# Kernel tuning notes

Hardware: AMD Instinct MI355X
Metric: run time of the kernel (lower is better)

Reference implementation:

```python
import jax, jax.numpy as jnp
import numpy as np

WINDOW = 7
EPS = 1e-8


def setup_inputs() -> dict:
    key = jax.random.key(0)
    k1, k2, k3 = jax.random.split(key, 3)
    x = jax.random.normal(k1, (8, 256, 64, 64), dtype=jnp.float32)
    # 1x1 conv weights (bias=False): [out_ch, in_ch]
    w_reduce = jax.random.normal(k2, (64, 256), dtype=jnp.float32) * 0.05
    w_proj = jax.random.normal(k3, (512, 64), dtype=jnp.float32) * 0.1
    return {"x": x, "w_reduce": w_reduce, "w_proj": w_proj}


def _unfold_window(feat, window):
    # feat: [b, c, h, w] -> patches: [b, c, window*window, h, w]
    b, c, h, w = feat.shape
    pad = window // 2
    fp = jnp.pad(feat, ((0, 0), (0, 0), (pad, pad), (pad, pad)))
    # fixed small loop over window^2 = 49 shifts (matches F.unfold ordering)
    return jnp.stack(
        [fp[:, :, i:i + h, j:j + w] for i in range(window) for j in range(window)],
        axis=2,
    )


def reference(x, w_reduce, w_proj):
    window = WINDOW
    # reduce: 1x1 conv, no bias
    feat = jnp.einsum('oc,bchw->bohw', w_reduce, x)  # [b, cr, h, w]
    patches = _unfold_window(feat, window)           # [b, cr, K, h, w], K=49
    # cosine similarity between center feature and each window patch (dim=channel)
    dot = jnp.einsum('bchw,bckhw->bkhw', feat, patches)          # [b, K, h, w]
    cn = jnp.sqrt(jnp.sum(feat * feat, axis=1))                  # [b, h, w]
    pn = jnp.sqrt(jnp.sum(patches * patches, axis=1))            # [b, K, h, w]
    sim = dot / jnp.maximum(cn[:, None] * pn, EPS)               # [b, K, h, w]
    att = jax.nn.softmax(sim, axis=1)                            # softmax over window dim
    corr = jnp.einsum('bkhw,bckhw->bchw', att, patches)          # [b, cr, h, w]
    # proj: 1x1 conv, no bias
    return jnp.einsum('oc,bchw->bohw', w_proj, corr)             # [b, out, h, w]
```

## Files before the change

### kernel.cpp

```cpp
#include <hip/hip_runtime.h>
#include <stdint.h>

#define NPIX 4096
#define CIN  256
#define CR   64
#define COUT 512
#define NB   8
#define CG   256
#define FT   128

typedef _Float16 half8 __attribute__((ext_vector_type(8)));
typedef _Float16 half4 __attribute__((ext_vector_type(4)));
typedef _Float16 half2v __attribute__((ext_vector_type(2)));
typedef float f32x4 __attribute__((ext_vector_type(4)));

__device__ __forceinline__ float dpp8_sum(float d) {
  int y;
  y = __builtin_amdgcn_update_dpp(0, __float_as_int(d), 0xB1, 0xF, 0xF, true);
  d += __int_as_float(y);
  y = __builtin_amdgcn_update_dpp(0, __float_as_int(d), 0x4E, 0xF, 0xF, true);
  d += __int_as_float(y);
  y = __builtin_amdgcn_update_dpp(0, __float_as_int(d), 0x141, 0xF, 0xF, true);
  d += __int_as_float(y);
  return d;
}

__global__ __launch_bounds__(256) void k0_prep(
    const float* __restrict__ wr, const float* __restrict__ wp,
    _Float16* __restrict__ wrAh, _Float16* __restrict__ wrAl,
    _Float16* __restrict__ wpH,
    float* __restrict__ icnG, float* __restrict__ featTail)
{
  const int tid = blockIdx.x * 256 + threadIdx.x;
  if (tid < 16384) {
    const int j = tid & 7, l = (tid >> 3) & 63;
    const int kt = (tid >> 9) & 7, mt = tid >> 12;
    const int m = mt * 16 + (l & 15);
    const int k = kt * 32 + (l >> 4) * 8 + j;
    const float v = wr[m * CIN + k];
    const _Float16 h = (_Float16)v;
    wrAh[tid] = h;
    wrAl[tid] = (_Float16)(v - (float)h);
  } else if (tid < 16384 + COUT * CR) {
    const int fi = tid - 16384;
    const int j = fi & 7, l = (fi >> 3) & 63;
    const int kt = (fi >> 9) & 1, ot = (fi >> 10) & 3, g = fi >> 12;
    const int o = g * 64 + ot * 16 + (l & 15);
    const int k = kt * 32 + (l >> 4) * 8 + j;
    wpH[fi] = (_Float16)wp[o * CR + k];
  } else {
    const int gi = tid - (16384 + COUT * CR);
    if (gi < CG)               icnG[gi] = 0.f;
    else if (gi < 2 * CG)      icnG[CG + NB * NPIX + (gi - CG)] = 0.f;
    else if (gi < 2 * CG + FT) featTail[gi - 2 * CG] = 0.f;
  }
}

__global__ __launch_bounds__(512) void k1_reduce(
    const float* __restrict__ x,
    const _Float16* __restrict__ wrAh, const _Float16* __restrict__ wrAl,
    _Float16* __restrict__ feat_h, float* __restrict__ icn)
{
  const int blk = blockIdx.x;
  const int b = blk >> 6, seg = blk & 63;
  const int t = threadIdx.x, lane = t & 63;
  const int g = __builtin_amdgcn_readfirstlane((int)t >> 6);
  const int nt = g & 3, mth = g >> 2;
  const int col = lane & 15, krow = lane >> 4;

  const float* xb = x + (size_t)b * CIN * NPIX + seg * 64 + nt * 16 + col;

  f32x4 c0 = {0.f, 0.f, 0.f, 0.f};
  f32x4 c1 = {0.f, 0.f, 0.f, 0.f};

#pragma unroll
  for (int kt = 0; kt < 8; ++kt) {
    half8 Bh, Bl;
    const float* xk = xb + (size_t)(kt * 32 + krow * 8) * NPIX;
#pragma unroll
    for (int j = 0; j < 8; ++j) {
      const float v = xk[(size_t)j * NPIX];
      const _Float16 h = (_Float16)v;
      Bh[j] = h;
      Bl[j] = (_Float16)(v - (float)h);
    }
    const int fi0 = ((mth * 2 + 0) * 8 + kt) * 512 + lane * 8;
    const int fi1 = ((mth * 2 + 1) * 8 + kt) * 512 + lane * 8;
    const half8 Ah0 = *(const half8*)(wrAh + fi0);
    const half8 Al0 = *(const half8*)(wrAl + fi0);
    const half8 Ah1 = *(const half8*)(wrAh + fi1);
    const half8 Al1 = *(const half8*)(wrAl + fi1);
    c0 = __builtin_amdgcn_mfma_f32_16x16x32_f16(Ah0, Bh, c0, 0, 0, 0);
    c0 = __builtin_amdgcn_mfma_f32_16x16x32_f16(Ah0, Bl, c0, 0, 0, 0);
    c0 = __builtin_amdgcn_mfma_f32_16x16x32_f16(Al0, Bh, c0, 0, 0, 0);
    c1 = __builtin_amdgcn_mfma_f32_16x16x32_f16(Ah1, Bh, c1, 0, 0, 0);
    c1 = __builtin_amdgcn_mfma_f32_16x16x32_f16(Ah1, Bl, c1, 0, 0, 0);
    c1 = __builtin_amdgcn_mfma_f32_16x16x32_f16(Al1, Bh, c1, 0, 0, 0);
  }

  const int px = seg * 64 + nt * 16 + col;
  _Float16* fb = feat_h + ((size_t)b * NPIX + px) * 64;
  const int ch0 = mth * 32 + krow * 4;
  half4 v0, v1;
  float p = 0.f;
#pragma unroll
  for (int r = 0; r < 4; ++r) {
    v0[r] = (_Float16)c0[r];
    v1[r] = (_Float16)c1[r];
    p = fmaf(c0[r], c0[r], p);
    p = fmaf(c1[r], c1[r], p);
  }
  *(half4*)(fb + ch0) = v0;
  *(half4*)(fb + ch0 + 16) = v1;

  p += __shfl_xor(p, 16);
  p += __shfl_xor(p, 32);

  __shared__ float cn[8][16];
  if (lane < 16) cn[g][lane] = p;
  __syncthreads();
  if (t < 64) {
    const int nt2 = t >> 4, c16 = t & 15;
    const float ss = cn[nt2][c16] + cn[nt2 + 4][c16];
    icn[b * NPIX + seg * 64 + t] = rsqrtf(fmaxf(ss, 1e-16f));
  }
}

__global__ __launch_bounds__(512, 4) void k23_fused(
    const _Float16* __restrict__ feat_h, const float* __restrict__ icn,
    const _Float16* __restrict__ wpH, float* __restrict__ out)
{
  const int blk = blockIdx.x;
  const int b = blk & 7, h = blk >> 3;
  const int t = threadIdx.x;
  const int lane = t & 63;
  const int g = __builtin_amdgcn_readfirstlane((int)t >> 6);
  const int w = t >> 3;
  const int cb = (t & 7) * 8;
  const int px = h * 64 + w;
  const int gpx = b * NPIX + px;

  const float* cnb = icn + b * NPIX;

  __shared__ __align__(16) _Float16 fs[2][72][72];
  __shared__ float cnS[2][80];
  __shared__ __align__(16) _Float16 corrH[4096];

  half8 rS0, rS1;
  float rc = 0.f;

  auto LOAD = [&](int ar) {
    const long rowb = ((long)b * NPIX + ar * 64 - 4) * 64;
    rS0 = *(const half8*)(feat_h + rowb + (long)t * 8);
    if (t < 64) rS1 = *(const half8*)(feat_h + rowb + (long)(512 + t) * 8);
    if (t < 72) rc = cnb[ar * 64 - 4 + t];
  };
  auto WRITE = [&](int bufi) {
    *(half8*)&fs[bufi][t >> 3][(t & 7) * 8] = rS0;
    if (t < 64) *(half8*)&fs[bufi][64 + (t >> 3)][(t & 7) * 8] = rS1;
    if (t < 72) cnS[bufi][t] = rc;
  };

  half2v fc2[4];
  {
    const half8 fcv = *(const half8*)(feat_h + ((size_t)b * NPIX + px) * 64 + cb);
#pragma unroll
    for (int i = 0; i < 4; ++i) { fc2[i][0] = fcv[2*i]; fc2[i][1] = fcv[2*i+1]; }
  }
  const float icnc = icn[gpx];

  half2v accA[4], accB[4];
#pragma unroll
  for (int i = 0; i < 4; ++i) {
    accA[i] = (half2v)(_Float16)0.f;
    accB[i] = (half2v)(_Float16)0.f;
  }

  const int lo = (h - 3 < 0) ? 0 : h - 3;
  const int hi = (h + 3 > 63) ? 63 : h + 3;
  float l = 7.0f * (float)(6 - (hi - lo));

  LOAD(lo);
  WRITE(0);
  __syncthreads();

  int buf = 0;
  for (int ar = lo; ar <= hi; ++ar) {
    if (ar < hi) LOAD(ar + 1);
#pragma unroll
    for (int dx = -3; dx <= 3; ++dx) {
      const int j = w + 4 + dx;
      const half8 nv = *(const half8*)&fs[buf][j][cb];
      half2v n0, n1, n2, n3;
      n0[0] = nv[0]; n0[1] = nv[1];
      n1[0] = nv[2]; n1[1] = nv[3];
      n2[0] = nv[4]; n2[1] = nv[5];
      n3[0] = nv[6]; n3[1] = nv[7];
      float d = 0.f;
      d = __builtin_amdgcn_fdot2(fc2[0], n0, d, false);
      d = __builtin_amdgcn_fdot2(fc2[1], n1, d, false);
      d = __builtin_amdgcn_fdot2(fc2[2], n2, d, false);
      d = __builtin_amdgcn_fdot2(fc2[3], n3, d, false);
      d = dpp8_sum(d);
      const float icnk = cnS[buf][j];
      float sim = d * icnc * icnk;
      const bool valid = (unsigned)(w + dx) < 64u;
      sim = valid ? sim : 0.f;
      const float p = __expf(sim);
      l += p;
      const float pv = valid ? p : 0.f;
      const _Float16 ph = (_Float16)pv;
      half2v ph2; ph2[0] = ph; ph2[1] = ph;
      if (dx & 1) {
        accA[0] = ph2 * n0 + accA[0];
        accA[1] = ph2 * n1 + accA[1];
        accA[2] = ph2 * n2 + accA[2];
        accA[3] = ph2 * n3 + accA[3];
      } else {
        accB[0] = ph2 * n0 + accB[0];
        accB[1] = ph2 * n1 + accB[1];
        accB[2] = ph2 * n2 + accB[2];
        accB[3] = ph2 * n3 + accB[3];
      }
    }
    if (ar < hi) WRITE(buf ^ 1);
    __syncthreads();
    buf ^= 1;
  }

  {
    const float inv = __builtin_amdgcn_rcpf(l);
    half8 hv;
#pragma unroll
    for (int i = 0; i < 4; ++i) {
      const float a0 = (float)accA[i][0] + (float)accB[i][0];
      const float a1 = (float)accA[i][1] + (float)accB[i][1];
      hv[2*i]   = (_Float16)(a0 * inv);
      hv[2*i+1] = (_Float16)(a1 * inv);
    }
    const int wbyte = (w * 128 + (cb << 1)) ^ ((w & 7) << 4);
    *(half8*)((char*)corrH + wbyte) = hv;
  }
  __syncthreads();

  const _Float16* wA = wpH + (size_t)g * 4096;
  float* outb = out + ((size_t)b * COUT + g * 64) * NPIX + h * 64;
#pragma unroll
  for (int pt = 0; pt < 4; ++pt) {
    half8 Bf0, Bf1;
    {
      const int pxl = pt * 16 + (lane & 15);
      const int sw = (pxl & 7) << 4;
      const int rowb = pxl * 128 + ((lane >> 4) << 4);
      Bf0 = *(const half8*)((const char*)corrH + (rowb ^ sw));
      Bf1 = *(const half8*)((const char*)corrH + ((rowb + 64) ^ sw));
    }
#pragma unroll
    for (int ot = 0; ot < 4; ++ot) {
      f32x4 c = {0.f, 0.f, 0.f, 0.f};
      const half8 A0 = *(const half8*)(wA + (ot * 2 + 0) * 512 + lane * 8);
      const half8 A1 = *(const half8*)(wA + (ot * 2 + 1) * 512 + lane * 8);
      c = __builtin_amdgcn_mfma_f32_16x16x32_f16(A0, Bf0, c, 0, 0, 0);
      c = __builtin_amdgcn_mfma_f32_16x16x32_f16(A1, Bf1, c, 0, 0, 0);
      float* op = outb + (size_t)(ot * 16 + ((lane >> 4) << 2)) * NPIX
                       + pt * 16 + (lane & 15);
#pragma unroll
      for (int r = 0; r < 4; ++r) op[(size_t)r * NPIX] = c[r];
    }
  }
}

extern "C" void kernel_launch(void* const* d_in, const int* in_sizes, int n_in,
                              void* d_out, int out_size, void* d_ws, size_t ws_size,
                              hipStream_t stream)
{
  const float* x  = (const float*)d_in[0];
  const float* wr = (const float*)d_in[1];
  const float* wp = (const float*)d_in[2];
  float* out = (float*)d_out;

  float* ws = (float*)d_ws;
  _Float16* wrAh  = (_Float16*)ws;
  _Float16* wrAl  = (_Float16*)(ws + 8192);
  _Float16* wpH   = (_Float16*)(ws + 16384);
  float* icnG     = ws + 32768;
  float* icn      = icnG + CG;
  _Float16* feat_h = (_Float16*)(icn + NB * NPIX + CG);
  float* featTail = (float*)(feat_h + (size_t)NB * NPIX * 64);

  hipLaunchKernelGGL(k0_prep,   dim3(195), dim3(256), 0, stream, wr, wp, wrAh, wrAl, wpH, icnG, featTail);
  hipLaunchKernelGGL(k1_reduce, dim3(512), dim3(512), 0, stream, x, wrAh, wrAl, feat_h, icn);
  hipLaunchKernelGGL(k23_fused, dim3(512), dim3(512), 0, stream, feat_h, icn, wpH, out);
}
```

Before: 40.48 us.

## Process two output rows per block to share staged neighbor rows

The fused attention/projection kernel now runs 1024-thread blocks that each handle two adjacent image rows, streaming 8 feature rows through the shared double buffer instead of 7 per single row. This cuts redundant global-to-LDS staging of overlapping window rows and halves the block count. The projection weights are also preloaded into registers before the barrier. In exchange, each half-block idles during the boundary row it does not need, and register pressure rises under the 1024-thread launch bound, which may lower occupancy.

```diff
diff --git a/kernel.cpp b/kernel.cpp
--- a/kernel.cpp
+++ b/kernel.cpp
@@ -126,39 +126,41 @@
   }
 }
 
-__global__ __launch_bounds__(512, 4) void k23_fused(
+__global__ __launch_bounds__(1024, 4) void k23_fused(
     const _Float16* __restrict__ feat_h, const float* __restrict__ icn,
     const _Float16* __restrict__ wpH, float* __restrict__ out)
 {
   const int blk = blockIdx.x;
-  const int b = blk & 7, h = blk >> 3;
+  const int b = blk & 7, hh = blk >> 3;
+  const int h0 = hh * 2;
   const int t = threadIdx.x;
   const int lane = t & 63;
-  const int g = __builtin_amdgcn_readfirstlane((int)t >> 6);
-  const int w = t >> 3;
-  const int cb = (t & 7) * 8;
-  const int px = h * 64 + w;
+  const int wv = __builtin_amdgcn_readfirstlane((int)t >> 6);
+  const int half = wv >> 3;
+  const int tl = t & 511;
+  const int w = tl >> 3;
+  const int cb = (tl & 7) * 8;
+  const int rc = h0 + half;
+  const int px = rc * 64 + w;
   const int gpx = b * NPIX + px;
 
   const float* cnb = icn + b * NPIX;
 
   __shared__ __align__(16) _Float16 fs[2][72][72];
   __shared__ float cnS[2][80];
-  __shared__ __align__(16) _Float16 corrH[4096];
-
-  half8 rS0, rS1;
-  float rc = 0.f;
+  __shared__ __align__(16) _Float16 corrH[2][4096];
+
+  half8 rS0;
+  float ricn = 0.f;
 
   auto LOAD = [&](int ar) {
     const long rowb = ((long)b * NPIX + ar * 64 - 4) * 64;
-    rS0 = *(const half8*)(feat_h + rowb + (long)t * 8);
-    if (t < 64) rS1 = *(const half8*)(feat_h + rowb + (long)(512 + t) * 8);
-    if (t < 72) rc = cnb[ar * 64 - 4 + t];
+    if (t < 576) rS0 = *(const half8*)(feat_h + rowb + (long)t * 8);
+    if (t < 72) ricn = cnb[ar * 64 - 4 + t];
   };
   auto WRITE = [&](int bufi) {
-    *(half8*)&fs[bufi][t >> 3][(t & 7) * 8] = rS0;
-    if (t < 64) *(half8*)&fs[bufi][64 + (t >> 3)][(t & 7) * 8] = rS1;
-    if (t < 72) cnS[bufi][t] = rc;
+    if (t < 576) *(half8*)&fs[bufi][t >> 3][(t & 7) * 8] = rS0;
+    if (t < 72) cnS[bufi][t] = ricn;
   };
 
   half2v fc2[4];
@@ -176,54 +178,59 @@
     accB[i] = (half2v)(_Float16)0.f;
   }
 
-  const int lo = (h - 3 < 0) ? 0 : h - 3;
-  const int hi = (h + 3 > 63) ? 63 : h + 3;
-  float l = 7.0f * (float)(6 - (hi - lo));
-
-  LOAD(lo);
+  const int lo_r = (rc - 3 < 0) ? 0 : rc - 3;
+  const int hi_r = (rc + 3 > 63) ? 63 : rc + 3;
+  float l = 7.0f * (float)(6 - (hi_r - lo_r));
+
+  const int blo = (h0 - 3 < 0) ? 0 : h0 - 3;
+  const int bhi = (h0 + 4 > 63) ? 63 : h0 + 4;
+
+  LOAD(blo);
   WRITE(0);
   __syncthreads();
 
   int buf = 0;
-  for (int ar = lo; ar <= hi; ++ar) {
-    if (ar < hi) LOAD(ar + 1);
-#pragma unroll
-    for (int dx = -3; dx <= 3; ++dx) {
-      const int j = w + 4 + dx;
-      const half8 nv = *(const half8*)&fs[buf][j][cb];
-      half2v n0, n1, n2, n3;
-      n0[0] = nv[0]; n0[1] = nv[1];
-      n1[0] = nv[2]; n1[1] = nv[3];
-      n2[0] = nv[4]; n2[1] = nv[5];
-      n3[0] = nv[6]; n3[1] = nv[7];
-      float d = 0.f;
-      d = __builtin_amdgcn_fdot2(fc2[0], n0, d, false);
-      d = __builtin_amdgcn_fdot2(fc2[1], n1, d, false);
-      d = __builtin_amdgcn_fdot2(fc2[2], n2, d, false);
-      d = __builtin_amdgcn_fdot2(fc2[3], n3, d, false);
-      d = dpp8_sum(d);
-      const float icnk = cnS[buf][j];
-      float sim = d * icnc * icnk;
-      const bool valid = (unsigned)(w + dx) < 64u;
-      sim = valid ? sim : 0.f;
-      const float p = __expf(sim);
-      l += p;
-      const float pv = valid ? p : 0.f;
-      const _Float16 ph = (_Float16)pv;
-      half2v ph2; ph2[0] = ph; ph2[1] = ph;
-      if (dx & 1) {
-        accA[0] = ph2 * n0 + accA[0];
-        accA[1] = ph2 * n1 + accA[1];
-        accA[2] = ph2 * n2 + accA[2];
-        accA[3] = ph2 * n3 + accA[3];
-      } else {
-        accB[0] = ph2 * n0 + accB[0];
-        accB[1] = ph2 * n1 + accB[1];
-        accB[2] = ph2 * n2 + accB[2];
-        accB[3] = ph2 * n3 + accB[3];
+  for (int ar = blo; ar <= bhi; ++ar) {
+    if (ar < bhi) LOAD(ar + 1);
+    if (ar >= lo_r && ar <= hi_r) {
+#pragma unroll
+      for (int dx = -3; dx <= 3; ++dx) {
+        const int j = w + 4 + dx;
+        const half8 nv = *(const half8*)&fs[buf][j][cb];
+        half2v n0, n1, n2, n3;
+        n0[0] = nv[0]; n0[1] = nv[1];
+        n1[0] = nv[2]; n1[1] = nv[3];
+        n2[0] = nv[4]; n2[1] = nv[5];
+        n3[0] = nv[6]; n3[1] = nv[7];
+        float d = 0.f;
+        d = __builtin_amdgcn_fdot2(fc2[0], n0, d, false);
+        d = __builtin_amdgcn_fdot2(fc2[1], n1, d, false);
+        d = __builtin_amdgcn_fdot2(fc2[2], n2, d, false);
+        d = __builtin_amdgcn_fdot2(fc2[3], n3, d, false);
+        d = dpp8_sum(d);
+        const float icnk = cnS[buf][j];
+        float sim = d * icnc * icnk;
+        const bool valid = (unsigned)(w + dx) < 64u;
+        sim = valid ? sim : 0.f;
+        const float p = __expf(sim);
+        l += p;
+        const float pv = valid ? p : 0.f;
+        const _Float16 ph = (_Float16)pv;
+        half2v ph2; ph2[0] = ph; ph2[1] = ph;
+        if (dx & 1) {
+          accA[0] = ph2 * n0 + accA[0];
+          accA[1] = ph2 * n1 + accA[1];
+          accA[2] = ph2 * n2 + accA[2];
+          accA[3] = ph2 * n3 + accA[3];
+        } else {
+          accB[0] = ph2 * n0 + accB[0];
+          accB[1] = ph2 * n1 + accB[1];
+          accB[2] = ph2 * n2 + accB[2];
+          accB[3] = ph2 * n3 + accB[3];
+        }
       }
     }
-    if (ar < hi) WRITE(buf ^ 1);
+    if (ar < bhi) WRITE(buf ^ 1);
     __syncthreads();
     buf ^= 1;
   }
@@ -239,12 +246,18 @@
       hv[2*i+1] = (_Float16)(a1 * inv);
     }
     const int wbyte = (w * 128 + (cb << 1)) ^ ((w & 7) << 4);
-    *(half8*)((char*)corrH + wbyte) = hv;
-  }
+    *(half8*)((char*)&corrH[half][0] + wbyte) = hv;
+  }
+
+  const _Float16* wA = wpH + (size_t)(wv & 7) * 4096;
+  half8 Af[8];
+#pragma unroll
+  for (int e = 0; e < 8; ++e) Af[e] = *(const half8*)(wA + e * 512 + lane * 8);
   __syncthreads();
 
-  const _Float16* wA = wpH + (size_t)g * 4096;
-  float* outb = out + ((size_t)b * COUT + g * 64) * NPIX + h * 64;
+  const char* cH = (const char*)&corrH[wv >> 3][0];
+  float* outb = out + ((size_t)b * COUT + (wv & 7) * 64) * NPIX
+              + (h0 + (wv >> 3)) * 64;
 #pragma unroll
   for (int pt = 0; pt < 4; ++pt) {
     half8 Bf0, Bf1;
@@ -252,16 +265,14 @@
       const int pxl = pt * 16 + (lane & 15);
       const int sw = (pxl & 7) << 4;
       const int rowb = pxl * 128 + ((lane >> 4) << 4);
-      Bf0 = *(const half8*)((const char*)corrH + (rowb ^ sw));
-      Bf1 = *(const half8*)((const char*)corrH + ((rowb + 64) ^ sw));
+      Bf0 = *(const half8*)(cH + (rowb ^ sw));
+      Bf1 = *(const half8*)(cH + ((rowb + 64) ^ sw));
     }
 #pragma unroll
     for (int ot = 0; ot < 4; ++ot) {
       f32x4 c = {0.f, 0.f, 0.f, 0.f};
-      const half8 A0 = *(const half8*)(wA + (ot * 2 + 0) * 512 + lane * 8);
-      const half8 A1 = *(const half8*)(wA + (ot * 2 + 1) * 512 + lane * 8);
-      c = __builtin_amdgcn_mfma_f32_16x16x32_f16(A0, Bf0, c, 0, 0, 0);
-      c = __builtin_amdgcn_mfma_f32_16x16x32_f16(A1, Bf1, c, 0, 0, 0);
+      c = __builtin_amdgcn_mfma_f32_16x16x32_f16(Af[ot * 2 + 0], Bf0, c, 0, 0, 0);
+      c = __builtin_amdgcn_mfma_f32_16x16x32_f16(Af[ot * 2 + 1], Bf1, c, 0, 0, 0);
       float* op = outb + (size_t)(ot * 16 + ((lane >> 4) << 2)) * NPIX
                        + pt * 16 + (lane & 15);
 #pragma unroll
@@ -290,5 +301,5 @@
 
   hipLaunchKernelGGL(k0_prep,   dim3(195), dim3(256), 0, stream, wr, wp, wrAh, wrAl, wpH, icnG, featTail);
   hipLaunchKernelGGL(k1_reduce, dim3(512), dim3(512), 0, stream, x, wrAh, wrAl, feat_h, icn);
-  hipLaunchKernelGGL(k23_fused, dim3(512), dim3(512), 0, stream, feat_h, icn, wpH, out);
-}
+  hipLaunchKernelGGL(k23_fused, dim3(256), dim3(1024), 0, stream, feat_h, icn, wpH, out);
+}
```

Result: slower. 42.22 us (+4.3%).

## Split fused attention+proj kernel into half-row blocks of 256 threads

Applied to the files above, without the earlier changes.

The fused correlation/projection kernel now processes half an image row (32 pixels) per block with 256 threads, doubling the grid to 1024 blocks. Each block stages a 40-pixel halo window in shared memory instead of 72, and each wave computes 8 output-channel tiles over 2 pixel tiles in the projection GEMM. This is meant to raise occupancy and spread work across more CUs, at the cost of more redundant halo loads and each wave reading more projection weights.

```diff
diff --git a/kernel.cpp b/kernel.cpp
--- a/kernel.cpp
+++ b/kernel.cpp
@@ -126,39 +126,42 @@
   }
 }
 
-__global__ __launch_bounds__(512, 4) void k23_fused(
+__global__ __launch_bounds__(256, 4) void k23_fused(
     const _Float16* __restrict__ feat_h, const float* __restrict__ icn,
     const _Float16* __restrict__ wpH, float* __restrict__ out)
 {
   const int blk = blockIdx.x;
-  const int b = blk & 7, h = blk >> 3;
+  const int b = blk & 7;
+  const int rest = blk >> 3;
+  const int h = rest >> 1, s = rest & 1;
   const int t = threadIdx.x;
   const int lane = t & 63;
-  const int g = __builtin_amdgcn_readfirstlane((int)t >> 6);
+  const int wv = __builtin_amdgcn_readfirstlane((int)t >> 6);
   const int w = t >> 3;
   const int cb = (t & 7) * 8;
-  const int px = h * 64 + w;
+  const int wg = s * 32 + w;
+  const int px = h * 64 + wg;
   const int gpx = b * NPIX + px;
 
   const float* cnb = icn + b * NPIX;
 
-  __shared__ __align__(16) _Float16 fs[2][72][72];
-  __shared__ float cnS[2][80];
-  __shared__ __align__(16) _Float16 corrH[4096];
+  __shared__ __align__(16) _Float16 fs[2][40][72];
+  __shared__ float cnS[2][48];
+  __shared__ __align__(16) _Float16 corrH[2048];
 
   half8 rS0, rS1;
-  float rc = 0.f;
+  float ricn = 0.f;
 
   auto LOAD = [&](int ar) {
-    const long rowb = ((long)b * NPIX + ar * 64 - 4) * 64;
-    rS0 = *(const half8*)(feat_h + rowb + (long)t * 8);
-    if (t < 64) rS1 = *(const half8*)(feat_h + rowb + (long)(512 + t) * 8);
-    if (t < 72) rc = cnb[ar * 64 - 4 + t];
+    const long base = ((long)b * NPIX + ar * 64 + s * 32 - 4) * 64;
+    rS0 = *(const half8*)(feat_h + base + (long)t * 8);
+    if (t < 64) rS1 = *(const half8*)(feat_h + base + (long)(256 + t) * 8);
+    if (t < 40) ricn = cnb[ar * 64 + s * 32 - 4 + t];
   };
   auto WRITE = [&](int bufi) {
     *(half8*)&fs[bufi][t >> 3][(t & 7) * 8] = rS0;
-    if (t < 64) *(half8*)&fs[bufi][64 + (t >> 3)][(t & 7) * 8] = rS1;
-    if (t < 72) cnS[bufi][t] = rc;
+    if (t < 64) *(half8*)&fs[bufi][32 + (t >> 3)][(t & 7) * 8] = rS1;
+    if (t < 40) cnS[bufi][t] = ricn;
   };
 
   half2v fc2[4];
@@ -204,7 +207,7 @@
       d = dpp8_sum(d);
       const float icnk = cnS[buf][j];
       float sim = d * icnc * icnk;
-      const bool valid = (unsigned)(w + dx) < 64u;
+      const bool valid = (unsigned)(wg + dx) < 64u;
       sim = valid ? sim : 0.f;
       const float p = __expf(sim);
       l += p;
@@ -243,27 +246,27 @@
   }
   __syncthreads();
 
-  const _Float16* wA = wpH + (size_t)g * 4096;
-  float* outb = out + ((size_t)b * COUT + g * 64) * NPIX + h * 64;
-#pragma unroll
-  for (int pt = 0; pt < 4; ++pt) {
+  const char* cH = (const char*)corrH;
+#pragma unroll
+  for (int pt = 0; pt < 2; ++pt) {
     half8 Bf0, Bf1;
     {
       const int pxl = pt * 16 + (lane & 15);
       const int sw = (pxl & 7) << 4;
       const int rowb = pxl * 128 + ((lane >> 4) << 4);
-      Bf0 = *(const half8*)((const char*)corrH + (rowb ^ sw));
-      Bf1 = *(const half8*)((const char*)corrH + ((rowb + 64) ^ sw));
-    }
-#pragma unroll
-    for (int ot = 0; ot < 4; ++ot) {
+      Bf0 = *(const half8*)(cH + (rowb ^ sw));
+      Bf1 = *(const half8*)(cH + ((rowb + 64) ^ sw));
+    }
+#pragma unroll
+    for (int ot = 0; ot < 8; ++ot) {
+      const int T = wv * 8 + ot;
       f32x4 c = {0.f, 0.f, 0.f, 0.f};
-      const half8 A0 = *(const half8*)(wA + (ot * 2 + 0) * 512 + lane * 8);
-      const half8 A1 = *(const half8*)(wA + (ot * 2 + 1) * 512 + lane * 8);
+      const half8 A0 = *(const half8*)(wpH + (size_t)(T * 2 + 0) * 512 + lane * 8);
+      const half8 A1 = *(const half8*)(wpH + (size_t)(T * 2 + 1) * 512 + lane * 8);
       c = __builtin_amdgcn_mfma_f32_16x16x32_f16(A0, Bf0, c, 0, 0, 0);
       c = __builtin_amdgcn_mfma_f32_16x16x32_f16(A1, Bf1, c, 0, 0, 0);
-      float* op = outb + (size_t)(ot * 16 + ((lane >> 4) << 2)) * NPIX
-                       + pt * 16 + (lane & 15);
+      float* op = out + ((size_t)b * COUT + T * 16 + ((lane >> 4) << 2)) * NPIX
+                      + h * 64 + s * 32 + pt * 16 + (lane & 15);
 #pragma unroll
       for (int r = 0; r < 4; ++r) op[(size_t)r * NPIX] = c[r];
     }
@@ -288,7 +291,7 @@
   _Float16* feat_h = (_Float16*)(icn + NB * NPIX + CG);
   float* featTail = (float*)(feat_h + (size_t)NB * NPIX * 64);
 
-  hipLaunchKernelGGL(k0_prep,   dim3(195), dim3(256), 0, stream, wr, wp, wrAh, wrAl, wpH, icnG, featTail);
-  hipLaunchKernelGGL(k1_reduce, dim3(512), dim3(512), 0, stream, x, wrAh, wrAl, feat_h, icn);
-  hipLaunchKernelGGL(k23_fused, dim3(512), dim3(512), 0, stream, feat_h, icn, wpH, out);
-}
+  hipLaunchKernelGGL(k0_prep,   dim3(195),  dim3(256), 0, stream, wr, wp, wrAh, wrAl, wpH, icnG, featTail);
+  hipLaunchKernelGGL(k1_reduce, dim3(512),  dim3(512), 0, stream, x, wrAh, wrAl, feat_h, icn);
+  hipLaunchKernelGGL(k23_fused, dim3(1024), dim3(256), 0, stream, feat_h, icn, wpH, out);
+}
```

Result: no change. 39.79 us (-1.7%).
